# Kernel tuning notes

Measured on AMD Instinct MI355X. Metric: run time of the kernel, lower is better.

Reference implementation:

```python
import jax, jax.numpy as jnp
import numpy as np

S, B, D = 2048, 16, 512  # seq_len, batch, dim_in (= value_dim = key_dim)


def setup_inputs() -> dict:
    key = jax.random.key(0)
    ks = jax.random.split(key, 7)
    scale = 1.0 / np.sqrt(D)
    return {
        "seq": jax.random.normal(ks[0], (S, B, D), dtype=jnp.float32),
        "Wv": jax.random.normal(ks[1], (D, D), dtype=jnp.float32) * scale,
        "bv": jax.random.normal(ks[2], (D,), dtype=jnp.float32) * 0.01,
        "Wq": jax.random.normal(ks[3], (D, D), dtype=jnp.float32) * scale,
        "bq": jax.random.normal(ks[4], (D,), dtype=jnp.float32) * 0.01,
        "Wk": jax.random.normal(ks[5], (D, D), dtype=jnp.float32) * scale,
        "bk": jax.random.normal(ks[6], (D,), dtype=jnp.float32) * 0.01,
    }


def reference(seq, Wv, bv, Wq, bq, Wk, bk):
    # seq: [S, B, D] -> [B, S, D]
    x = jnp.transpose(seq, (1, 0, 2))
    value = x @ Wv.T + bv   # [B, S, Dv]
    query = x @ Wq.T + bq   # [B, S, Dv]
    keys = x @ Wk.T + bk    # [B, S, Dk]
    inv_sqrt_d = 1.0 / np.sqrt(seq.shape[-1]).astype(np.float32)
    # note: scores use value @ query^T (roles swapped vs standard SDPA), per source
    weights = jnp.einsum('bsd,btd->bst', value, query) * inv_sqrt_d  # [B, S, S]
    weights = jax.nn.softmax(weights, axis=-1)
    out = jnp.einsum('bst,btk->bsk', weights, keys)  # [B, S, Dk]
    return jnp.transpose(out, (1, 0, 2))  # [S, B, Dk]
```

## Files before the change

### kernel.cpp

```cpp
#include <hip/hip_runtime.h>
#include <hip/hip_bf16.h>

#define SS 2048
#define BB 16
#define DD 512

typedef __attribute__((ext_vector_type(4))) float f32x4;
typedef __attribute__((ext_vector_type(8))) short bf16x8;
typedef __attribute__((ext_vector_type(4))) unsigned short us4;
typedef unsigned short us;

#define MFMA16(a,b,c) __builtin_amdgcn_mfma_f32_16x16x32_bf16((a),(b),(c),0,0,0)
#define BAR() __builtin_amdgcn_s_barrier()
#define WAITV(n) asm volatile("s_waitcnt vmcnt(" #n ")" ::: "memory")
#define WAITL()  asm volatile("s_waitcnt lgkmcnt(0)" ::: "memory")

__device__ __forceinline__ unsigned short f2b(float f) {
    union { float f; unsigned u; } v; v.f = f;
    unsigned r = v.u + 0x7FFFu + ((v.u >> 16) & 1u);
    return (unsigned short)(r >> 16);
}

__device__ __forceinline__ bf16x8 ldfrag8(const us* base, int row, int kelem) {
    int off = (row << 8) + (kelem << 1);
    off ^= (row & 15) << 4;
    return *(const bf16x8*)((const char*)base + off);
}
__device__ __forceinline__ bf16x8 ldfrag(const us* base, int row, int kelem, int rowshift) {
    int off = (row << rowshift) + (kelem << 1);
    off ^= (row & 7) << 4;
    return *(const bf16x8*)((const char*)base + off);
}

__device__ __forceinline__ void gl16(const void* g, void* l) {
    __builtin_amdgcn_global_load_lds(
        (const __attribute__((address_space(1))) unsigned*)g,
        (__attribute__((address_space(3))) unsigned*)l, 16, 0, 0);
}

__global__ __launch_bounds__(256) void k_prep_x(const float* __restrict__ seq,
        us* __restrict__ Xb, us* __restrict__ Xbt) {
    __shared__ __align__(16) char L[64 * 128];
    const int tid = threadIdx.x;
    const int d0 = blockIdx.x * 64, s0 = blockIdx.y * 64, b = blockIdx.z;
    {
        int r = tid >> 2, seg = (tid & 3) * 16;
        const float* src = seq + (size_t)(s0 + r) * (BB * DD) + (size_t)b * DD + d0 + seg;
        __align__(16) us vals[16];
        #pragma unroll
        for (int q = 0; q < 4; ++q) {
            f32x4 v = *(const f32x4*)(src + q * 4);
            vals[q*4+0] = f2b(v.x); vals[q*4+1] = f2b(v.y);
            vals[q*4+2] = f2b(v.z); vals[q*4+3] = f2b(v.w);
        }
        us* xo = Xb + ((size_t)b * SS + s0 + r) * DD + d0 + seg;
        *(bf16x8*)xo       = *(bf16x8*)&vals[0];
        *(bf16x8*)(xo + 8) = *(bf16x8*)&vals[8];
        #pragma unroll
        for (int j = 0; j < 16; ++j) {
            int d = seg + j;
            int addr = (d * 128 + r * 2) ^ ((d & 7) << 4);
            *(us*)(L + addr) = vals[j];
        }
    }
    __syncthreads();
    {
        int d = tid >> 2, sseg = (tid & 3) * 16;
        int c = (d & 7) << 4;
        int base = d * 128 + sseg * 2;
        bf16x8 h0 = *(bf16x8*)(L + (base ^ c));
        bf16x8 h1 = *(bf16x8*)(L + ((base + 16) ^ c));
        us* o = Xbt + ((size_t)b * DD + d0 + d) * SS + s0 + sseg;
        *(bf16x8*)o       = h0;
        *(bf16x8*)(o + 8) = h1;
    }
}

__global__ __launch_bounds__(256) void k_prepG(const float* __restrict__ Wv,
        const float* __restrict__ Wq, us* __restrict__ Gt) {
    __shared__ float Sq[32][64], Sv[32][64];
    const int tid = threadIdx.x;
    const int p0 = blockIdx.x * 64, i0 = blockIdx.y * 64;
    const int tp = tid & 15, ti = tid >> 4;
    float acc[4][4] = {};
    for (int a0 = 0; a0 < DD; a0 += 32) {
        #pragma unroll
        for (int j = 0; j < 2; ++j) {
            int slot = tid + j * 256;
            int row = slot >> 4, c4 = (slot & 15) * 4;
            *(f32x4*)&Sq[row][c4] = *(const f32x4*)(Wq + (size_t)(a0 + row) * DD + p0 + c4);
            *(f32x4*)&Sv[row][c4] = *(const f32x4*)(Wv + (size_t)(a0 + row) * DD + i0 + c4);
        }
        __syncthreads();
        for (int a = 0; a < 32; ++a) {
            f32x4 q = *(f32x4*)&Sq[a][tp * 4];
            f32x4 v = *(f32x4*)&Sv[a][ti * 4];
            #pragma unroll
            for (int x = 0; x < 4; ++x)
                #pragma unroll
                for (int y = 0; y < 4; ++y)
                    acc[x][y] += q[x] * v[y];
        }
        __syncthreads();
    }
    const float sc = 0.044194173824159216f;
    #pragma unroll
    for (int x = 0; x < 4; ++x)
        #pragma unroll
        for (int y = 0; y < 4; ++y)
            Gt[(size_t)(p0 + tp * 4 + x) * DD + i0 + ti * 4 + y] = f2b(acc[x][y] * sc);
}

__global__ __launch_bounds__(512) void k_prepU(const float* __restrict__ Wq,
        const float* __restrict__ bv, float* __restrict__ u) {
    int p = threadIdx.x;
    float s = 0.f;
    for (int a0 = 0; a0 < DD; a0 += 8) {
        #pragma unroll
        for (int j = 0; j < 8; ++j)
            s += bv[a0 + j] * Wq[(size_t)(a0 + j) * DD + p];
    }
    u[p] = s * 0.044194173824159216f;
}

__global__ void k_prepW(const float* __restrict__ Wk, us* __restrict__ Wkb) {
    int i = (blockIdx.x * 256 + threadIdx.x) * 4;
    f32x4 v = *(const f32x4*)(Wk + i);
    us4 o; o.x = f2b(v.x); o.y = f2b(v.y); o.z = f2b(v.z); o.w = f2b(v.w);
    *(us4*)(Wkb + i) = o;
}

template<int MODE>
__global__ __launch_bounds__(256, 2) void k_bgemm(
        const us* __restrict__ A, const us* __restrict__ Bm,
        const float* __restrict__ bias, float* __restrict__ Ls,
        void* __restrict__ outp,
        int K, int lda, int ldb, int ldc,
        long aStr, long bStr, long oStr,
        int aB, int bB, int oB, int lsB) {
    __shared__ __align__(16) us As[2][128 * 64];
    __shared__ __align__(16) us Bs[2][128 * 64];
    const int tid = threadIdx.x;
    const int lane = tid & 63;
    const int w = tid >> 6;
    const int wr = w >> 1, wc = w & 1;
    const int l15 = lane & 15, lg = lane >> 4;
    const int s0 = blockIdx.x * 128;
    const int n0 = blockIdx.y * 128;
    const int za = aB + blockIdx.z, zb = bB + blockIdx.z;
    const int zo = oB + blockIdx.z, zl = lsB + blockIdx.z;
    const char* abase = (const char*)(A + (size_t)za * aStr + (size_t)s0 * lda);
    const char* bbase = (const char*)(Bm + (size_t)zb * bStr + (size_t)n0 * ldb);
    const size_t arow = (size_t)lda * 2, brow = (size_t)ldb * 2;

    f32x4 acc[4][4];
    #pragma unroll
    for (int m = 0; m < 4; ++m)
        #pragma unroll
        for (int n = 0; n < 4; ++n) acc[m][n] = (f32x4)(0.0f);

    auto stage = [&](int db, int p) {
        #pragma unroll
        for (int j = 0; j < 4; ++j) {
            int x = (tid + j * 256) * 16;
            int gx = x ^ (((x >> 7) & 7) << 4);
            int row = gx >> 7, col = gx & 127;
            gl16(abase + (size_t)row * arow + p * 128 + col, (char*)As[db] + x);
            gl16(bbase + (size_t)row * brow + p * 128 + col, (char*)Bs[db] + x);
        }
    };

    const int nPh = K >> 6;
    stage(0, 0);
    for (int p = 0; p < nPh; ++p) {
        if (p < nPh - 1) { stage((p + 1) & 1, p + 1); WAITV(8); }
        else             { WAITV(0); }
        BAR();
        const us* Ac = As[p & 1]; const us* Bc = Bs[p & 1];
        __builtin_amdgcn_s_setprio(1);
        #pragma unroll
        for (int kk = 0; kk < 2; ++kk) {
            bf16x8 af[4], bfr[4];
            #pragma unroll
            for (int m = 0; m < 4; ++m) af[m]  = ldfrag(Ac, 64 * wr + 16 * m + l15, kk * 32 + 8 * lg, 7);
            #pragma unroll
            for (int n = 0; n < 4; ++n) bfr[n] = ldfrag(Bc, 64 * wc + 16 * n + l15, kk * 32 + 8 * lg, 7);
            #pragma unroll
            for (int m = 0; m < 4; ++m)
                #pragma unroll
                for (int n = 0; n < 4; ++n)
                    acc[m][n] = MFMA16(af[m], bfr[n], acc[m][n]);
        }
        __builtin_amdgcn_s_setprio(0);
        BAR();
    }

    if (MODE == 0) {
        us* o = (us*)outp + (size_t)zo * oStr;
        float rs[4][4];
        #pragma unroll
        for (int m = 0; m < 4; ++m)
            #pragma unroll
            for (int r = 0; r < 4; ++r) rs[m][r] = 0.0f;
        #pragma unroll
        for (int m = 0; m < 4; ++m)
            #pragma unroll
            for (int n = 0; n < 4; ++n) {
                int col = n0 + 64 * wc + 16 * n + l15;
                #pragma unroll
                for (int r = 0; r < 4; ++r) {
                    int row = s0 + 64 * wr + 16 * m + 4 * lg + r;
                    float pe = __expf(acc[m][n][r]);
                    rs[m][r] += pe;
                    o[(size_t)row * ldc + col] = f2b(pe);
                }
            }
        #pragma unroll
        for (int m = 0; m < 4; ++m)
            #pragma unroll
            for (int r = 0; r < 4; ++r) {
                float v = rs[m][r];
                v += __shfl_xor(v, 1); v += __shfl_xor(v, 2);
                v += __shfl_xor(v, 4); v += __shfl_xor(v, 8);
                if (l15 == 0)
                    atomicAdd(&Ls[(size_t)zl * SS + s0 + 64 * wr + 16 * m + 4 * lg + r], v);
            }
    } else if (MODE == 2) {
        float* o = (float*)outp;
        #pragma unroll
        for (int m = 0; m < 4; ++m)
            #pragma unroll
            for (int n = 0; n < 4; ++n) {
                int col = n0 + 64 * wc + 16 * n + l15;
                float bia = bias[col];
                #pragma unroll
                for (int r = 0; r < 4; ++r) {
                    int row = s0 + 64 * wr + 16 * m + 4 * lg + r;
                    float L = Ls[(size_t)zl * SS + row];
                    o[((size_t)row * BB + zo) * DD + col] = acc[m][n][r] / L + bia;
                }
            }
    } else {
        us* o = (us*)outp + (size_t)zo * oStr;
        #pragma unroll
        for (int m = 0; m < 4; ++m)
            #pragma unroll
            for (int n = 0; n < 4; ++n) {
                int col = n0 + 64 * wc + 16 * n + l15;
                float bia = (MODE == 3) ? bias[col] : 0.0f;
                #pragma unroll
                for (int r = 0; r < 4; ++r) {
                    int row = s0 + 64 * wr + 16 * m + 4 * lg + r;
                    o[(size_t)row * ldc + col] = f2b(acc[m][n][r] + bia);
                }
            }
    }
}

__global__ __launch_bounds__(512, 2) void k_attn(
        const us* __restrict__ Vtb, const us* __restrict__ Xb,
        const us* __restrict__ Xbt, us* __restrict__ Ob) {
    __shared__ __align__(16) us BUFS[4][16384];
    __shared__ __align__(16) us Pb[64 * 128];
    __shared__ float red[2][64];

    const int tid = threadIdx.x;
    const int lane = tid & 63;
    const int w = tid >> 6;
    const int rg = w & 3;
    const int cg = w >> 2;
    const int l15 = lane & 15, lg = lane >> 4;

    const int wg = blockIdx.x;
    const int b  = ((wg >> 8) << 3) | (wg & 7);
    const int s0 = ((wg >> 3) & 31) * 64;

    const char* vbase  = (const char*)(Vtb + ((size_t)b * SS + s0) * DD);
    const char* xabase = (const char*)(Xb  + (size_t)b * SS * DD);
    const char* xtbase = (const char*)(Xbt + (size_t)b * DD * SS);

    auto issue = [&](int cflat, us* dst0) {
        int c = cflat & 127;
        int i = c & 7, t0 = (c >> 3) << 7;
        char* dst = (char*)dst0;
        if (i < 4) {
            #pragma unroll
            for (int j = 0; j < 4; ++j) {
                int x = tid * 16 + j * 8192;
                int gx = x ^ (((x >> 8) & 15) << 4);
                int row = gx >> 8, col = gx & 255;
                gl16(xabase + (size_t)(t0 + row) * 1024 + i * 256 + col, dst + x);
            }
        } else {
            #pragma unroll
            for (int j = 0; j < 4; ++j) {
                int x = tid * 16 + j * 8192;
                int gx = x ^ (((x >> 8) & 15) << 4);
                int row = gx >> 8, col = gx & 255;
                gl16(xtbase + (size_t)((i - 4) * 128 + row) * (SS * 2)
                            + (size_t)t0 * 2 + col, dst + x);
            }
        }
    };

    #pragma unroll
    for (int p = 0; p < 4; ++p) {
        #pragma unroll
        for (int j = 0; j < 2; ++j) {
            int x = tid * 16 + j * 8192;
            int gx = x ^ (((x >> 8) & 15) << 4);
            int row = gx >> 8, col = gx & 255;
            gl16(vbase + (size_t)row * 1024 + p * 256 + col,
                 (char*)BUFS[0] + p * 16384 + x);
        }
    }
    WAITV(0); BAR();
    bf16x8 af[16];
    #pragma unroll
    for (int p = 0; p < 4; ++p)
        #pragma unroll
        for (int kk = 0; kk < 4; ++kk)
            af[4 * p + kk] = ldfrag8((const us*)BUFS[0] + p * 8192,
                                     16 * rg + l15, 32 * kk + 8 * lg);
    WAITL(); BAR();

    issue(0, BUFS[0]);
    issue(1, BUFS[1]);
    issue(2, BUFS[2]);

    f32x4 accv[4][4];
    #pragma unroll
    for (int ph = 0; ph < 4; ++ph)
        #pragma unroll
        for (int nt = 0; nt < 4; ++nt) accv[ph][nt] = (f32x4)(0.0f);
    float lsum[4] = {0.f, 0.f, 0.f, 0.f};
    const int idx = 16 * rg + 4 * lg;

    for (int step = 0; step < 16; ++step) {
        const int cbase = step * 8;
        f32x4 sacc[4];
        #pragma unroll
        for (int nt = 0; nt < 4; ++nt) sacc[nt] = (f32x4)(0.0f);

        #pragma unroll
        for (int p = 0; p < 4; ++p) {
            const int c = cbase + p;
            WAITV(8); BAR();
            const us* sl = BUFS[c & 3];
            __builtin_amdgcn_s_setprio(1);
            #pragma unroll
            for (int kk = 0; kk < 4; ++kk)
                #pragma unroll
                for (int nt = 0; nt < 4; ++nt) {
                    bf16x8 bq = ldfrag8(sl, 64 * cg + 16 * nt + l15, 32 * kk + 8 * lg);
                    sacc[nt] = MFMA16(af[4 * p + kk], bq, sacc[nt]);
                }
            __builtin_amdgcn_s_setprio(0);
            issue(c + 3, BUFS[(c + 3) & 3]);
        }

        #pragma unroll
        for (int nt = 0; nt < 4; ++nt)
            #pragma unroll
            for (int ri = 0; ri < 4; ++ri)
                sacc[nt][ri] = __expf(sacc[nt][ri]);
        #pragma unroll
        for (int nt = 0; nt < 4; ++nt)
            #pragma unroll
            for (int ri = 0; ri < 4; ++ri) {
                int row = idx + ri;
                int col = 64 * cg + 16 * nt + l15;
                int off = ((row << 8) + (col << 1)) ^ ((row & 15) << 4);
                *(us*)((char*)Pb + off) = f2b(sacc[nt][ri]);
            }
        #pragma unroll
        for (int ri = 0; ri < 4; ++ri) {
            float s = sacc[0][ri] + sacc[1][ri] + sacc[2][ri] + sacc[3][ri];
            s += __shfl_xor(s, 1); s += __shfl_xor(s, 2);
            s += __shfl_xor(s, 4); s += __shfl_xor(s, 8);
            lsum[ri] += s;
        }
        WAITL(); BAR();
        bf16x8 pa[4];
        #pragma unroll
        for (int kk = 0; kk < 4; ++kk)
            pa[kk] = ldfrag8(Pb, 16 * rg + l15, 32 * kk + 8 * lg);

        #pragma unroll
        for (int p = 0; p < 4; ++p) {
            const int c = cbase + 4 + p;
            WAITV(8); BAR();
            const us* sl = BUFS[c & 3];
            __builtin_amdgcn_s_setprio(1);
            #pragma unroll
            for (int kk = 0; kk < 4; ++kk)
                #pragma unroll
                for (int nt = 0; nt < 4; ++nt) {
                    bf16x8 bx = ldfrag8(sl, 64 * cg + 16 * nt + l15, 32 * kk + 8 * lg);
                    accv[p][nt] = MFMA16(pa[kk], bx, accv[p][nt]);
                }
            __builtin_amdgcn_s_setprio(0);
            issue(c + 3, BUFS[(c + 3) & 3]);
        }
    }

    WAITV(0);
    if (l15 == 0) {
        #pragma unroll
        for (int ri = 0; ri < 4; ++ri)
            red[cg][idx + ri] = lsum[ri];
    }
    WAITL(); BAR();
    float tot[4];
    #pragma unroll
    for (int ri = 0; ri < 4; ++ri)
        tot[ri] = red[0][idx + ri] + red[1][idx + ri];
    us* orow = Ob + ((size_t)b * SS + s0) * DD;
    #pragma unroll
    for (int ph = 0; ph < 4; ++ph)
        #pragma unroll
        for (int nt = 0; nt < 4; ++nt)
            #pragma unroll
            for (int ri = 0; ri < 4; ++ri) {
                int row = idx + ri;
                int e = 128 * ph + 64 * cg + 16 * nt + l15;
                orow[(size_t)row * DD + e] = f2b(accv[ph][nt][ri] / tot[ri]);
            }
}

extern "C" void kernel_launch(void* const* d_in, const int* in_sizes, int n_in,
                              void* d_out, int out_size, void* d_ws, size_t ws_size,
                              hipStream_t stream) {
    const float* seq = (const float*)d_in[0];
    const float* Wv  = (const float*)d_in[1];
    const float* bv  = (const float*)d_in[2];
    const float* Wq  = (const float*)d_in[3];
    const float* Wk  = (const float*)d_in[5];
    const float* bk  = (const float*)d_in[6];

    char* ws = (char*)d_ws;
    us*    Xb  = (us*)ws;
    us*    Xbt = (us*)(ws + (size_t)33554432);
    us*    Vtb = (us*)(ws + (size_t)67108864);
    us*    Gt  = (us*)(ws + (size_t)100663296);
    us*    Wkb = (us*)(ws + (size_t)101187584);
    float* u   = (float*)(ws + (size_t)101711872);
    float* Ls  = (float*)(ws + (size_t)101713920);
    const size_t POFF = 101844992ull;
    us*    P   = (us*)(ws + POFF);

    long gb = 0;
    if (ws_size > POFF) {
        size_t cap = ws_size - POFF;
        for (long g = 16; g >= 1; g >>= 1)
            if ((size_t)g * SS * SS * 2 <= cap) { gb = g; break; }
    }

    k_prep_x<<<dim3(8, 32, 16), 256, 0, stream>>>(seq, Xb, Xbt);
    k_prepG<<<dim3(8, 8), 256, 0, stream>>>(Wv, Wq, Gt);
    k_prepU<<<1, 512, 0, stream>>>(Wq, bv, u);
    k_prepW<<<256, 256, 0, stream>>>(Wk, Wkb);

    k_bgemm<3><<<dim3(16, 4, 16), 256, 0, stream>>>(
        Xb, Gt, u, nullptr, (void*)Vtb,
        512, 512, 512, 512, (long)SS * DD, 0, (long)SS * DD, 0, 0, 0, 0);

    if (gb >= 1) {
        hipMemsetAsync(Ls, 0, (size_t)BB * SS * 4, stream);
        for (int g = 0; g < 16; g += (int)gb) {
            k_bgemm<0><<<dim3(16, 16, (int)gb), 256, 0, stream>>>(
                Vtb, Xb, nullptr, Ls, (void*)P,
                512, 512, 512, 2048, (long)SS * DD, (long)SS * DD, (long)SS * SS,
                g, g, 0, g);
            k_bgemm<1><<<dim3(16, 4, (int)gb), 256, 0, stream>>>(
                P, Xbt, nullptr, nullptr, (void*)Vtb,
                2048, 2048, 2048, 512, (long)SS * SS, (long)DD * SS, (long)SS * DD,
                0, g, g, 0);
        }
        k_bgemm<2><<<dim3(16, 4, 16), 256, 0, stream>>>(
            Vtb, Wkb, bk, Ls, d_out,
            512, 512, 512, 512, (long)SS * DD, 0, 0, 0, 0, 0, 0);
    } else {
        k_attn<<<512, 512, 0, stream>>>(Vtb, Xb, Xbt, Vtb);
        k_bgemm<2><<<dim3(16, 4, 16), 256, 0, stream>>>(
            Vtb, Wkb, bk, nullptr, d_out,
            512, 512, 512, 512, (long)SS * DD, 0, 0, 0, 0, 0, 0);
    }
}
```

Baseline: 343.9 us.

## Compute softmax row sums via ones-MFMA in PV GEMM instead of atomics

The softmax denominator is now accumulated inside the P·X GEMM (mode 1) by running extra MFMAs of the P fragments against a bf16 ones vector. It is written directly to Ls, which removes the shuffle reductions, global atomics and the memset from the exp epilogue. This adds about 25% more MFMA work in the PV GEMM, and every column block redundantly writes the same sums. The maximum batch group size also drops from 16 to 8, and the fallback path gets a no-normalisation output mode so it no longer reads a null Ls.

```diff
diff --git a/kernel.cpp b/kernel.cpp
--- a/kernel.cpp
+++ b/kernel.cpp
@@ -153,11 +153,18 @@
     const char* bbase = (const char*)(Bm + (size_t)zb * bStr + (size_t)n0 * ldb);
     const size_t arow = (size_t)lda * 2, brow = (size_t)ldb * 2;
 
+    const short one_bf = (short)0x3F80;
+    const bf16x8 ones = {one_bf, one_bf, one_bf, one_bf,
+                         one_bf, one_bf, one_bf, one_bf};
+
     f32x4 acc[4][4];
     #pragma unroll
     for (int m = 0; m < 4; ++m)
         #pragma unroll
         for (int n = 0; n < 4; ++n) acc[m][n] = (f32x4)(0.0f);
+    f32x4 lsum[4];
+    #pragma unroll
+    for (int m = 0; m < 4; ++m) lsum[m] = (f32x4)(0.0f);
 
     auto stage = [&](int db, int p) {
         #pragma unroll
@@ -190,6 +197,11 @@
                 #pragma unroll
                 for (int n = 0; n < 4; ++n)
                     acc[m][n] = MFMA16(af[m], bfr[n], acc[m][n]);
+            if (MODE == 1) {
+                #pragma unroll
+                for (int m = 0; m < 4; ++m)
+                    lsum[m] = MFMA16(af[m], ones, lsum[m]);
+            }
         }
         __builtin_amdgcn_s_setprio(0);
         BAR();
@@ -197,11 +209,6 @@
 
     if (MODE == 0) {
         us* o = (us*)outp + (size_t)zo * oStr;
-        float rs[4][4];
-        #pragma unroll
-        for (int m = 0; m < 4; ++m)
-            #pragma unroll
-            for (int r = 0; r < 4; ++r) rs[m][r] = 0.0f;
         #pragma unroll
         for (int m = 0; m < 4; ++m)
             #pragma unroll
@@ -210,22 +217,10 @@
                 #pragma unroll
                 for (int r = 0; r < 4; ++r) {
                     int row = s0 + 64 * wr + 16 * m + 4 * lg + r;
-                    float pe = __expf(acc[m][n][r]);
-                    rs[m][r] += pe;
-                    o[(size_t)row * ldc + col] = f2b(pe);
+                    o[(size_t)row * ldc + col] = f2b(__expf(acc[m][n][r]));
                 }
             }
-        #pragma unroll
-        for (int m = 0; m < 4; ++m)
-            #pragma unroll
-            for (int r = 0; r < 4; ++r) {
-                float v = rs[m][r];
-                v += __shfl_xor(v, 1); v += __shfl_xor(v, 2);
-                v += __shfl_xor(v, 4); v += __shfl_xor(v, 8);
-                if (l15 == 0)
-                    atomicAdd(&Ls[(size_t)zl * SS + s0 + 64 * wr + 16 * m + 4 * lg + r], v);
-            }
-    } else if (MODE == 2) {
+    } else if (MODE == 2 || MODE == 4) {
         float* o = (float*)outp;
         #pragma unroll
         for (int m = 0; m < 4; ++m)
@@ -236,8 +231,9 @@
                 #pragma unroll
                 for (int r = 0; r < 4; ++r) {
                     int row = s0 + 64 * wr + 16 * m + 4 * lg + r;
-                    float L = Ls[(size_t)zl * SS + row];
-                    o[((size_t)row * BB + zo) * DD + col] = acc[m][n][r] / L + bia;
+                    float v = acc[m][n][r];
+                    if (MODE == 2) v /= Ls[(size_t)zl * SS + row];
+                    o[((size_t)row * BB + zo) * DD + col] = v + bia;
                 }
             }
     } else {
@@ -254,6 +250,14 @@
                     o[(size_t)row * ldc + col] = f2b(acc[m][n][r] + bia);
                 }
             }
+        if (MODE == 1) {
+            #pragma unroll
+            for (int m = 0; m < 4; ++m)
+                #pragma unroll
+                for (int r = 0; r < 4; ++r)
+                    if (l15 == 0)
+                        Ls[(size_t)zl * SS + s0 + 64 * wr + 16 * m + 4 * lg + r] = lsum[m][r];
+        }
     }
 }
 
@@ -452,7 +456,7 @@
     long gb = 0;
     if (ws_size > POFF) {
         size_t cap = ws_size - POFF;
-        for (long g = 16; g >= 1; g >>= 1)
+        for (long g = 8; g >= 1; g >>= 1)
             if ((size_t)g * SS * SS * 2 <= cap) { gb = g; break; }
     }
 
@@ -466,23 +470,22 @@
         512, 512, 512, 512, (long)SS * DD, 0, (long)SS * DD, 0, 0, 0, 0);
 
     if (gb >= 1) {
-        hipMemsetAsync(Ls, 0, (size_t)BB * SS * 4, stream);
         for (int g = 0; g < 16; g += (int)gb) {
             k_bgemm<0><<<dim3(16, 16, (int)gb), 256, 0, stream>>>(
-                Vtb, Xb, nullptr, Ls, (void*)P,
+                Vtb, Xb, nullptr, nullptr, (void*)P,
                 512, 512, 512, 2048, (long)SS * DD, (long)SS * DD, (long)SS * SS,
-                g, g, 0, g);
+                g, g, 0, 0);
             k_bgemm<1><<<dim3(16, 4, (int)gb), 256, 0, stream>>>(
-                P, Xbt, nullptr, nullptr, (void*)Vtb,
+                P, Xbt, nullptr, Ls, (void*)Vtb,
                 2048, 2048, 2048, 512, (long)SS * SS, (long)DD * SS, (long)SS * DD,
-                0, g, g, 0);
+                0, g, g, g);
         }
         k_bgemm<2><<<dim3(16, 4, 16), 256, 0, stream>>>(
             Vtb, Wkb, bk, Ls, d_out,
             512, 512, 512, 512, (long)SS * DD, 0, 0, 0, 0, 0, 0);
     } else {
         k_attn<<<512, 512, 0, stream>>>(Vtb, Xb, Xbt, Vtb);
-        k_bgemm<2><<<dim3(16, 4, 16), 256, 0, stream>>>(
+        k_bgemm<4><<<dim3(16, 4, 16), 256, 0, stream>>>(
             Vtb, Wkb, bk, nullptr, d_out,
             512, 512, 512, 512, (long)SS * DD, 0, 0, 0, 0, 0, 0);
     }
```

Measured after the change: 326.8 us. 5.0% less time.
